# Kernel optimization log

Hardware: AMD Instinct MI355X
Metric: run time of the kernel (lower is better)

Reference implementation:

```python
import jax, jax.numpy as jnp
import numpy as np

B, L, H, W = 16, 4096, 64, 64
SEQ = 1024  # target_sequence_length (hardcoded in the torch module)
SP = 32     # sqrt(SEQ)


def _conv1d(x, w, b, pad):
    y = jax.lax.conv_general_dilated(x, w, (1,), [(pad, pad)],
                                     dimension_numbers=('NCH', 'OIH', 'NCH'))
    return y + b[None, :, None]


def _conv2d(x, w, b, pad, groups=1):
    y = jax.lax.conv_general_dilated(x, w, (1, 1), [(pad, pad)] * 2,
                                     feature_group_count=groups,
                                     dimension_numbers=('NCHW', 'OIHW', 'NCHW'))
    return y + b[None, :, None, None]


def _forward(us_input, img_input, us_w1, us_b1, us_w2, us_b2, us_w3, us_b3,
             aff_w, aff_w_high, aff_thr, img_w1, img_b1, img_w2, img_b2, img_w3, img_b3,
             db_qkv_w, db_qkv_b, db_dw_w, db_dw_b, db_proj_w, db_proj_b,
             db_fc_w, db_fc_b, db_dep_w, db_dep_b, db_temp,
             ca_qkv_w, ca_qkv_b, ca_out_w, ca_out_b,
             tf_ch1_w, tf_ch1_b, tf_ch2_w, tf_ch2_b,
             tf_sp1_w, tf_sp1_b, tf_sp2_w, tf_sp2_b, cls_w, cls_b):
    b = us_input.shape[0]
    # ---- ultrasound 1D conv branch ----
    x = us_input.transpose(0, 2, 1)                    # [B,1,L]
    x = jax.nn.relu(_conv1d(x, us_w1, us_b1, 1))
    x = jax.nn.relu(_conv1d(x, us_w2, us_b2, 1))
    x = jax.nn.relu(_conv1d(x, us_w3, us_b3, 1))
    us_feat = x.transpose(0, 2, 1)                     # [B,L,64]
    # ---- adaptive frequency filtering (training-mode high-freq mask included) ----
    n = us_feat.shape[1]
    xf = jnp.fft.rfft(us_feat, axis=1, norm='ortho')   # [B,Nf,64] complex
    w_c = aff_w[:, 0] + 1j * aff_w[:, 1]
    xw = xf * w_c
    energy = jnp.sum(jnp.abs(xf) ** 2, axis=-1)        # [B,Nf]
    med = jnp.median(energy.reshape(b, -1), axis=1, keepdims=True)
    ne = energy / (med + 1e-6)
    hard = (ne > aff_thr).astype(jnp.float32)
    mask = jax.lax.stop_gradient(hard - aff_thr) + aff_thr  # straight-through threshold
    wh_c = aff_w_high[:, 0] + 1j * aff_w_high[:, 1]
    xw = xw + (xf * mask[..., None]) * wh_c
    us_feat = jnp.fft.irfft(xw, n=n, axis=1, norm='ortho')  # [B,L,64]
    # ---- image 2D conv branch ----
    y = jax.nn.relu(_conv2d(img_input, img_w1, img_b1, 1))
    y = jax.nn.relu(_conv2d(y, img_w2, img_b2, 1))
    y = jax.nn.relu(_conv2d(y, img_w3, img_b3, 1))     # [B,64,H,W]
    # ---- dual-branch feature fusion block ----
    hgt, wid = y.shape[2], y.shape[3]
    hw = hgt * wid
    qkv = jnp.einsum('oi,bihw->bohw', db_qkv_w, y) + db_qkv_b[None, :, None, None]
    qkv = _conv2d(qkv, db_dw_w, db_dw_b, 1, groups=192)      # depthwise (3x3x3 conv @ D=1 -> center 3x3)
    # convolutional branch: faithful row-major reshape as in torch
    f_all = qkv.reshape(b, hw, 12, 16).transpose(0, 2, 1, 3)  # [B,12,HW,16]
    f_all = jnp.einsum('oi,bink->bonk', db_fc_w, f_all) + db_fc_b[None, :, None, None]
    f_conv = f_all.transpose(0, 3, 1, 2).reshape(b, 144, hgt, wid)
    out_conv = _conv2d(f_conv, db_dep_w, db_dep_b, 1, groups=16)  # [B,64,H,W]
    # channel attention branch
    q, k, v = jnp.split(qkv, 3, axis=1)
    q = q.reshape(b, 4, 16, hw)
    k = k.reshape(b, 4, 16, hw)
    v = v.reshape(b, 4, 16, hw)
    q = q / jnp.maximum(jnp.linalg.norm(q, axis=-1, keepdims=True), 1e-12)
    k = k / jnp.maximum(jnp.linalg.norm(k, axis=-1, keepdims=True), 1e-12)
    attn = jax.nn.softmax(jnp.einsum('bhcn,bhdn->bhcd', q, k) * db_temp, axis=-1)
    out = jnp.einsum('bhcd,bhdn->bhcn', attn, v).reshape(b, 64, hgt, wid)
    out = jnp.einsum('oi,bihw->bohw', db_proj_w, out) + db_proj_b[None, :, None, None]
    img_feat = (out + out_conv).reshape(b, 64, hw).transpose(0, 2, 1)  # [B,HW,64]
    # ---- adaptive avg pool to SEQ (lengths divide evenly) ----
    us_red = us_feat.transpose(0, 2, 1).reshape(b, 64, SEQ, -1).mean(-1).transpose(0, 2, 1)
    img_red = img_feat.transpose(0, 2, 1).reshape(b, 64, SEQ, -1).mean(-1).transpose(0, 2, 1)
    # ---- cross-modal attention (shared qkv/out projections) ----
    def heads(t):
        u = (jnp.einsum('bli,oi->blo', t, ca_qkv_w) + ca_qkv_b).reshape(b, SEQ, 4, 3, 16)
        return (u[:, :, :, 0].transpose(0, 2, 1, 3),
                u[:, :, :, 1].transpose(0, 2, 1, 3),
                u[:, :, :, 2].transpose(0, 2, 1, 3))
    q1, k1, v1 = heads(us_red)
    q2, k2, v2 = heads(img_red)
    scale = 1.0 / jnp.sqrt(jnp.float32(16.0))
    a1 = jax.nn.softmax(jnp.einsum('bhqd,bhkd->bhqk', q1, k2) * scale, axis=-1)
    a2 = jax.nn.softmax(jnp.einsum('bhqd,bhkd->bhqk', q2, k1) * scale, axis=-1)
    o1 = jnp.einsum('bhqk,bhkd->bhqd', a1, v2).transpose(0, 2, 1, 3).reshape(b, SEQ, 64)
    o2 = jnp.einsum('bhqk,bhkd->bhqd', a2, v1).transpose(0, 2, 1, 3).reshape(b, SEQ, 64)
    o1 = jnp.einsum('bli,oi->blo', o1, ca_out_w) + ca_out_b
    o2 = jnp.einsum('bli,oi->blo', o2, ca_out_w) + ca_out_b
    t1 = o1.transpose(0, 2, 1).reshape(b, 64, SP, SP)
    t2 = o2.transpose(0, 2, 1).reshape(b, 64, SP, SP)
    # ---- modal fusion attention (channel + spatial gating) ----
    ch_pool = jnp.stack([t1.mean((2, 3)), t1.max((2, 3)), t2.mean((2, 3)), t2.max((2, 3))], axis=1)  # [B,4,64]
    c1 = _conv1d(ch_pool, tf_ch1_w, tf_ch1_b, 1)      # [B,1,64]
    c2 = _conv1d(ch_pool, tf_ch2_w, tf_ch2_b, 1)
    ch_stack = jax.nn.softmax(jnp.stack([c1, c2], 0), axis=0)      # [2,B,1,64]
    ch_stack = ch_stack.transpose(0, 1, 3, 2)[..., None]           # [2,B,64,1,1]
    sp_pool = jnp.concatenate([t1.mean(1, keepdims=True), t1.max(1, keepdims=True),
                               t2.mean(1, keepdims=True), t2.max(1, keepdims=True)], axis=1)
    s1 = _conv2d(sp_pool, tf_sp1_w, tf_sp1_b, 3)
    s2 = _conv2d(sp_pool, tf_sp2_w, tf_sp2_b, 3)
    sp_stack = jax.nn.softmax(jnp.stack([s1, s2], 0), axis=0)      # [2,B,1,SP,SP]
    att = ch_stack + sp_stack + 1.0                                # [2,B,64,SP,SP]
    fuse = att[0] * t1 + att[1] * t2
    logits = fuse.mean((2, 3)) @ cls_w.T + cls_b
    return jax.nn.softmax(logits, axis=1)


def setup_inputs() -> dict:
    key = jax.random.key(0)
    ks = iter(jax.random.split(key, 64))
    def rn(shape, s=0.2):
        return jax.random.normal(next(ks), shape, dtype=jnp.float32) * s
    d = {
        'us_input': jax.random.normal(next(ks), (B, L, 1), dtype=jnp.float32),
        'img_input': jax.random.normal(next(ks), (B, 3, H, W), dtype=jnp.float32),
        'us_w1': rn((16, 1, 3)), 'us_b1': rn((16,), 0.02),
        'us_w2': rn((32, 16, 3)), 'us_b2': rn((32,), 0.02),
        'us_w3': rn((64, 32, 3)), 'us_b3': rn((64,), 0.02),
        'aff_w': rn((64, 2), 0.02), 'aff_w_high': rn((64, 2), 0.02),
        'aff_thr': jax.random.uniform(next(ks), (1,), dtype=jnp.float32),
        'img_w1': rn((16, 3, 3, 3)), 'img_b1': rn((16,), 0.02),
        'img_w2': rn((32, 16, 3, 3)), 'img_b2': rn((32,), 0.02),
        'img_w3': rn((64, 32, 3, 3)), 'img_b3': rn((64,), 0.02),
        'db_qkv_w': rn((192, 64), 0.1), 'db_qkv_b': rn((192,), 0.02),
        'db_dw_w': rn((192, 1, 3, 3)), 'db_dw_b': rn((192,), 0.02),
        'db_proj_w': rn((64, 64), 0.1), 'db_proj_b': rn((64,), 0.02),
        'db_fc_w': rn((9, 12), 0.1), 'db_fc_b': rn((9,), 0.02),
        'db_dep_w': rn((64, 9, 3, 3), 0.1), 'db_dep_b': rn((64,), 0.02),
        'db_temp': jnp.ones((4, 1, 1), dtype=jnp.float32),
        'ca_qkv_w': rn((192, 64), 0.1), 'ca_qkv_b': rn((192,), 0.02),
        'ca_out_w': rn((64, 64), 0.1), 'ca_out_b': rn((64,), 0.02),
        'tf_ch1_w': rn((1, 4, 3)), 'tf_ch1_b': rn((1,), 0.02),
        'tf_ch2_w': rn((1, 4, 3)), 'tf_ch2_b': rn((1,), 0.02),
        'tf_sp1_w': rn((1, 4, 7, 7)), 'tf_sp1_b': rn((1,), 0.02),
        'tf_sp2_w': rn((1, 4, 7, 7)), 'tf_sp2_b': rn((1,), 0.02),
        'cls_w': rn((9, 64), 0.1), 'cls_b': rn((9,), 0.02),
    }
    return d


def reference(us_input, img_input, us_w1, us_b1, us_w2, us_b2, us_w3, us_b3,
              aff_w, aff_w_high, aff_thr, img_w1, img_b1, img_w2, img_b2, img_w3, img_b3,
              db_qkv_w, db_qkv_b, db_dw_w, db_dw_b, db_proj_w, db_proj_b,
              db_fc_w, db_fc_b, db_dep_w, db_dep_b, db_temp,
              ca_qkv_w, ca_qkv_b, ca_out_w, ca_out_b,
              tf_ch1_w, tf_ch1_b, tf_ch2_w, tf_ch2_b,
              tf_sp1_w, tf_sp1_b, tf_sp2_w, tf_sp2_b, cls_w, cls_b):
    return _forward(us_input, img_input, us_w1, us_b1, us_w2, us_b2, us_w3, us_b3,
                    aff_w, aff_w_high, aff_thr, img_w1, img_b1, img_w2, img_b2, img_w3, img_b3,
                    db_qkv_w, db_qkv_b, db_dw_w, db_dw_b, db_proj_w, db_proj_b,
                    db_fc_w, db_fc_b, db_dep_w, db_dep_b, db_temp,
                    ca_qkv_w, ca_qkv_b, ca_out_w, ca_out_b,
                    tf_ch1_w, tf_ch1_b, tf_ch2_w, tf_ch2_b,
                    tf_sp1_w, tf_sp1_b, tf_sp2_w, tf_sp2_b, cls_w, cls_b)
```

## Files before the change

kernel.cpp:

```cpp
#include <hip/hip_runtime.h>

typedef float v2f __attribute__((ext_vector_type(2)));

static constexpr size_t O_SMALL   = 0;
static constexpr size_t O_US3     = 3145728;
static constexpr size_t O_XF      = 7340032;
static constexpr size_t O_USFILT  = 11536384;
static constexpr size_t O_ENERGY  = 15730688;
static constexpr size_t O_MED     = 15764480;
static constexpr size_t O_NRM     = 15765504;
static constexpr size_t O_ATTNS   = 15767552;
static constexpr size_t O_CHPOOL  = 15783936;
static constexpr size_t O_CHW     = 15788032;
static constexpr size_t O_SPPOOL  = 15790080;
static constexpr size_t O_SPW     = 15855616;
static constexpr size_t O_QKV     = 15888384;
static constexpr size_t O_QKVDW   = 28471296;
static constexpr size_t O_OUTCONV = 41054208;
static constexpr size_t CA_Q1 = 2, CA_K1 = 3, CA_V1 = 4,
                        CA_Q2 = 5, CA_K2 = 6, CA_V2 = 7, CA_O1 = 8, CA_O2 = 9,
                        CA_T1 = 10, CA_T2 = 11;


template<int Ci, int Co>
// ... 116 lines not shown
            float rev = (float)jm * cfac;
            float s1 = __builtin_amdgcn_sinf(rev);
            float c1 = __builtin_amdgcn_cosf(rev);
            float c2 = c1 * c1 - s1 * s1, s2 = 2.f * c1 * s1;
            float c3 = c2 * c1 - s2 * s1, s3 = c2 * s1 + s2 * c1;
            float2 v0 = va[r][0], v1 = va[r][1], v2 = va[r][2], v3 = va[r][3];
            float2 u1 = make_float2(v1.x * c1 - v1.y * s1, v1.x * s1 + v1.y * c1);
            float2 u2 = make_float2(v2.x * c2 - v2.y * s2, v2.x * s2 + v2.y * c2);
            float2 u3 = make_float2(v3.x * c3 - v3.y * s3, v3.x * s3 + v3.y * c3);
            float t0x = v0.x + u2.x, t0y = v0.y + u2.y;
            float t1x = v0.x - u2.x, t1y = v0.y - u2.y;
            float t2x = u1.x + u3.x, t2y = u1.y + u3.y;
            float t3x = u1.x - u3.x, t3y = u1.y - u3.y;
            int base = ((j - jm) << 2) + jm;
            A[base]          = make_float2(t0x + t2x, t0y + t2y);
            A[base + Ns]     = make_float2(t1x + t3y, t1y - t3x);
            A[base + 2 * Ns] = make_float2(t0x - t2x, t0y - t2y);
            A[base + 3 * Ns] = make_float2(t1x - t3y, t1y + t3x);
        }
        __syncthreads();
        Ns <<= 2;
    }
}

__device__ __forceinline__ void fft_fwd_body(char* smem_raw, int row,
    const float* __restrict__ us3, float* __restrict__ xf)
{
    float2* A = (float2*)smem_raw;
    int tid = threadIdx.x;
    const float* x = us3 + (size_t)row * 4096;
    for (int r = 0; r < 16; ++r) {
        int i = (r << 8) + tid;
        A[i] = make_float2(x[i], 0.f);
    }
    __syncthreads();
    fft4096_r4_sb(A, tid);
    float* out = xf + (size_t)row * 4098;
    for (int r = 0; r < 9; ++r) {
        int f = (r << 8) + tid;
        if (f < 2049) {
            out[2 * f]     = A[f].x * (1.f / 64.f);
            out[2 * f + 1] = A[f].y * (1.f / 64.f);
        }
    }
}

__device__ __forceinline__ void energy_body(int bid,
    const float* __restrict__ xf, float* __restrict__ energy)
{
    int idx = bid * 256 + threadIdx.x;
    if (idx >= 16 * 2049) return;
    int b = idx / 2049, f = idx % 2049;
    const float* p = xf + (size_t)b * 64 * 4098 + 2 * f;
    float e = 0.f;
    for (int ch = 0; ch < 64; ++ch) {
        float re = p[0], im = p[1];
        e += re * re + im * im;
        p += 4098;
    }
    energy[idx] = e;
}

__device__ __forceinline__ void median_body(char* smem_raw, int b,
    const float* __restrict__ energy, float* __restrict__ med)
{
    float* s = (float*)smem_raw;
    int tid = threadIdx.x;
    for (int r = 0; r < 16; ++r) {
        int i = (r << 8) + tid;
        s[i] = (i < 2049) ? energy[b * 2049 + i] : 3.0e38f;
    }
    __syncthreads();
    for (int k = 2; k <= 4096; k <<= 1) {
        for (int j = k >> 1; j > 0; j >>= 1) {
            for (int r = 0; r < 16; ++r) {
                int i = (r << 8) + tid;
                int ixj = i ^ j;
                if (ixj > i) {
                    bool up = ((i & k) == 0);
                    float a = s[i], bb = s[ixj];
                    if ((a > bb) == up) { s[i] = bb; s[ixj] = a; }
                }
            }
            __syncthreads();
        }
    }
    if (tid == 0) med[b] = s[1024];
}

__device__ __forceinline__ void filter_ifft_body(char* smem_raw, int row,
    const float* __restrict__ xf, const float* __restrict__ energy,
    const float* __restrict__ med, const float* __restrict__ aff_w,
    const float* __restrict__ aff_wh, const float* __restrict__ thr_p,
    float* __restrict__ us_redT)
{
    float2* A = (float2*)smem_raw;
    int b = row >> 6, ch = row & 63;
    int tid = threadIdx.x;
    float thr = thr_p[0];
    float mden = med[b] + 1e-6f;
    float w0r = aff_w[2 * ch], w0i = aff_w[2 * ch + 1];
    float whr = aff_wh[2 * ch], whi = aff_wh[2 * ch + 1];
    const float* X = xf + (size_t)row * 4098;
    const float* E = energy + b * 2049;
    for (int r = 0; r < 9; ++r) {
        int f = (r << 8) + tid;
        if (f < 2049) {
            float re = X[2 * f], im = X[2 * f + 1];
            float mask = (E[f] / mden > thr) ? 1.f : 0.f;
            float wr = w0r + mask * whr;
            float wi = w0i + mask * whi;
            float xr = re * wr - im * wi;
            float xi = re * wi + im * wr;
            A[f] = make_float2(xr, -xi);
            if (f >= 1 && f <= 2047) A[4096 - f] = make_float2(xr, xi);
        }
    }
    __syncthreads();
    fft4096_r4_sb(A, tid);
    float* outp = us_redT + (size_t)row * 1024;
    const float SCL = 0.25f * (1.f / 64.f);
#pragma unroll
    for (int r = 0; r < 4; ++r) {
        int s4 = (r << 8) + tid;
        float v = (A[4 * s4].x + A[4 * s4 + 1].x + A[4 * s4 + 2].x + A[4 * s4 + 3].x) * SCL;
        outp[s4] = v;
    }
}

__device__ __forceinline__ void qkv1x1_body(int bid, const float* __restrict__ y,
    const float* __restrict__ w, const float* __restrict__ bs, float* __restrict__ out)
{
    int oc = bid & 3;
    int pc = (bid >> 2) & 15;
    int b  = bid >> 6;
    int p = pc * 256 + threadIdx.x;
    const float* inb = y + (size_t)b * 262144 + p;
    v2f reg[32];
#pragma unroll
    for (int ci = 0; ci < 32; ++ci) {
        v2f r; r.x = inb[(2 * ci) * 4096]; r.y = inb[(2 * ci + 1) * 4096];
        reg[ci] = r;
    }
    float* ob = out + (size_t)b * 786432 + (size_t)oc * 48 * 4096 + p;
    for (int o = 0; o < 48; ++o) {
        const v2f* wr = (const v2f*)(w + (oc * 48 + o) * 64);
        v2f s2 = {0.f, 0.f};
#pragma unroll
        for (int ci = 0; ci < 32; ++ci) s2 = wr[ci] * reg[ci] + s2;
        ob[o * 4096] = bs[oc * 48 + o] + s2.x + s2.y;
    }
}

__device__ __forceinline__ void dwconv_body(int bid, const float* __restrict__ in,
    const float* __restrict__ w, const float* __restrict__ bs, float* __restrict__ out)
{
    int idx = bid * 256 + threadIdx.x;
    int x = idx & 63, yy = (idx >> 6) & 63;
    int c = (idx >> 12) % 192;
    const float* p = in + idx;
    const float* wp = w + c * 9;
    float acc = bs[c];
    bool ym = yy > 0, yp = yy < 63, xm = x > 0, xp = x < 63;
    float s = wp[4] * p[0];
    if (ym) { s += wp[1] * p[-64]; if (xm) s += wp[0] * p[-65]; if (xp) s += wp[2] * p[-63]; }
    if (xm) s += wp[3] * p[-1];
    if (xp) s += wp[5] * p[1];
    if (yp) { s += wp[7] * p[64];  if (xm) s += wp[6] * p[63];  if (xp) s += wp[8] * p[65]; }
    out[idx] = acc + s;
}

__device__ __forceinline__ void fc_body(int bid, const float* __restrict__ qkv_dw,
    const float* __restrict__ fw, const float* __restrict__ fb, float* __restrict__ fcv)
{
    int idx = bid * 256 + threadIdx.x;
    int k = idx & 15;
    int p = (idx >> 4) & 4095;
    int b = idx >> 16;
    const float* base = qkv_dw + (size_t)b * 786432;
    float u[12];
#pragma unroll
    for (int i = 0; i < 12; ++i) u[i] = base[p * 192 + i * 16 + k];
#pragma unroll
    for (int o = 0; o < 9; ++o) {
        float s = fb[o];
#pragma unroll
        for (int i = 0; i < 12; ++i) s += fw[o * 12 + i] * u[i];
        fcv[(((size_t)b * 16 + k) * 9 + o) * 4096 + p] = s;
    }
}

__device__ __forceinline__ void depconv2_body(char* smem_raw, int bid,
    const float* __restrict__ fcv, const float* __restrict__ w,
    const float* __restrict__ bs, float* __restrict__ out)
{
    auto lds = (float(*)[10][66])smem_raw;
    int band = bid & 7;
    int g    = (bid >> 3) & 15;
    int b    = bid >> 7;
    int y0 = band * 8;
    int tid = threadIdx.x;
    const float* inb = fcv + ((size_t)(b * 16 + g) * 9) * 4096;
    for (int i = tid; i < 9 * 10 * 64; i += 256) {
        int x  = i & 63;
        int ry = (i >> 6) % 10;
        int ci = i / 640;
        int gy = y0 - 1 + ry;
        lds[ci][ry][x + 1] = (gy >= 0 && gy < 64) ? inb[ci * 4096 + gy * 64 + x] : 0.f;
    }
    for (int i = tid; i < 90; i += 256) {
        int ry = i % 10, ci = i / 10;
        lds[ci][ry][0] = 0.f; lds[ci][ry][65] = 0.f;
    }
    __syncthreads();
    int co   = tid >> 6;
    int ysub = (tid >> 3) & 7;
    int x0   = (tid & 7) * 8;
    int ocg  = g * 4 + co;
    float acc[8];
    float bias = bs[ocg];
#pragma unroll
    for (int j = 0; j < 8; ++j) acc[j] = bias;
    const float* wb = w + ocg * 81;
    for (int ci = 0; ci < 9; ++ci) {
        float wr[9];
#pragma unroll
        for (int k = 0; k < 9; ++k) wr[k] = wb[ci * 9 + k];
#pragma unroll
        for (int dy = 0; dy < 3; ++dy) {
            const float* lr = &lds[ci][ysub + dy][x0];
            float a = lr[0], bb = lr[1];
#pragma unroll
            for (int j = 0; j < 8; ++j) {
                float cc = lr[2 + j];
                acc[j] += wr[dy * 3] * a + wr[dy * 3 + 1] * bb + wr[dy * 3 + 2] * cc;
                a = bb; bb = cc;
            }
        }
    }
    float* ob = out + ((size_t)b * 64 + ocg) * 4096 + (y0 + ysub) * 64 + x0;
#pragma unroll
    for (int j = 0; j < 8; ++j) ob[j] = acc[j];
}

__device__ __forceinline__ void qknorm_body(char* smem_raw, int row,
    const float* __restrict__ qkv_dw, float* __restrict__ nrm)
{
    float* red = (float*)smem_raw;
    int which = row >> 10;
    int r = row & 1023;
    int b = r >> 6, hd = r & 63;
    const float* p = qkv_dw + ((size_t)b * 192 + which * 64 + hd) * 4096;
    float s = 0.f;
    for (int i = threadIdx.x; i < 4096; i += 256) { float v = p[i]; s += v * v; }
    red[threadIdx.x] = s;
    __syncthreads();
    for (int st = 128; st > 0; st >>= 1) {
        if (threadIdx.x < st) red[threadIdx.x] += red[threadIdx.x + st];
        __syncthreads();
    }
    if (threadIdx.x == 0) nrm[row] = sqrtf(red[0]);
}

__device__ __forceinline__ void chan_attn_part_body(char* smem_raw, int blk,
    const float* __restrict__ qkv_dw, float* __restrict__ part)
{
    auto Qs  = (float(*)[130])smem_raw;
    auto Ks2 = (float(*)[130])(smem_raw + 16 * 130 * 4);
    int nc = blk & 7;
    int bh = blk >> 3;
    int b = bh >> 2, h = bh & 3;
    int c = threadIdx.x >> 4, d = threadIdx.x & 15;
    const float* qbase = qkv_dw + ((size_t)b * 192 + h * 16) * 4096 + nc * 512;
    const float* kbase = qkv_dw + ((size_t)b * 192 + 64 + h * 16) * 4096 + nc * 512;
    float s = 0.f;
    for (int n0 = 0; n0 < 512; n0 += 128) {
        __syncthreads();
        for (int r = 0; r < 8; ++r) {
            int i = (r << 8) + threadIdx.x;
            int row = i >> 7, col = i & 127;
            Qs[row][col]  = qbase[(size_t)row * 4096 + n0 + col];
            Ks2[row][col] = kbase[(size_t)row * 4096 + n0 + col];
        }
        __syncthreads();
#pragma unroll 8
        for (int n = 0; n < 128; ++n) s += Qs[c][n] * Ks2[d][n];
    }
    part[(size_t)blk * 256 + threadIdx.x] = s;
}

__device__ __forceinline__ void chpool2_body(int bid, const float* __restrict__ t1,
    const float* __restrict__ t2, float* __restrict__ chpool)
{
    int rg = bid & 15;
    int b  = bid >> 4;
    int wave = threadIdx.x >> 6, lane = threadIdx.x & 63;
    int c = rg * 4 + wave;
    const float* p1 = t1 + ((size_t)b * 64 + c) * 1024;
    const float* p2 = t2 + ((size_t)b * 64 + c) * 1024;
    float m1 = 0.f, x1 = -3e38f, m2 = 0.f, x2 = -3e38f;
#pragma unroll
    for (int i = 0; i < 16; ++i) {
        int p = lane + i * 64;
        float a = p1[p], bb = p2[p];
        m1 += a; x1 = fmaxf(x1, a);
        m2 += bb; x2 = fmaxf(x2, bb);
    }
    for (int off = 32; off > 0; off >>= 1) {
        m1 += __shfl_xor(m1, off);
        x1 = fmaxf(x1, __shfl_xor(x1, off));
        m2 += __shfl_xor(m2, off);
        x2 = fmaxf(x2, __shfl_xor(x2, off));
    }
    if (lane == 0) {
        chpool[b * 256 + c]       = m1 * (1.f / 1024.f);
        chpool[b * 256 + 64 + c]  = x1;
        chpool[b * 256 + 128 + c] = m2 * (1.f / 1024.f);
        chpool[b * 256 + 192 + c] = x2;
    }
}

__device__ __forceinline__ void sppool_body(int bid, const float* __restrict__ t1,
    const float* __restrict__ t2, float* __restrict__ sppool)
{
    int b = bid >> 2;
    int p = (bid & 3) * 256 + threadIdx.x;
    float m1 = 0.f, x1 = -3e38f, m2 = 0.f, x2 = -3e38f;
    const float* p1 = t1 + (size_t)b * 65536 + p;
    const float* p2 = t2 + (size_t)b * 65536 + p;
    for (int c = 0; c < 64; ++c) {
        float a = p1[c * 1024], bb = p2[c * 1024];
        m1 += a; x1 = fmaxf(x1, a);
        m2 += bb; x2 = fmaxf(x2, bb);
    }
    sppool[b * 4096 + p]        = m1 * (1.f / 64.f);
    sppool[b * 4096 + 1024 + p] = x1;
    sppool[b * 4096 + 2048 + p] = m2 * (1.f / 64.f);
    sppool[b * 4096 + 3072 + p] = x2;
}

__device__ __forceinline__ void chgate_body(int b, const float* __restrict__ chpool,
    const float* __restrict__ w1, const float* __restrict__ b1,
    const float* __restrict__ w2, const float* __restrict__ b2, float* __restrict__ chw)
{
    int c = threadIdx.x;
    if (c >= 64) return;
    float a1 = b1[0], a2 = b2[0];
    for (int ic = 0; ic < 4; ++ic) {
        const float* cp = chpool + b * 256 + ic * 64;
        for (int d = -1; d <= 1; ++d) {
            int cc = c + d;
            if (cc >= 0 && cc < 64) {
                a1 += w1[ic * 3 + d + 1] * cp[cc];
                a2 += w2[ic * 3 + d + 1] * cp[cc];
            }
        }
    }
    float mx = fmaxf(a1, a2);
    float e1 = __expf(a1 - mx), e2 = __expf(a2 - mx);
    float inv = 1.f / (e1 + e2);
    chw[b * 64 + c]        = e1 * inv;
    chw[1024 + b * 64 + c] = e2 * inv;
}

__device__ __forceinline__ void spgate_body(int bid, const float* __restrict__ sppool,
    const float* __restrict__ w1, const float* __restrict__ b1,
    const float* __restrict__ w2, const float* __restrict__ b2, float* __restrict__ spw)
{
    int idx = bid * 256 + threadIdx.x;
    int p = idx & 1023;
    int b = idx >> 10;
    int y = p >> 5, x = p & 31;
    float a1 = b1[0], a2 = b2[0];
    for (int ic = 0; ic < 4; ++ic) {
        const float* sp = sppool + b * 4096 + ic * 1024;
        for (int dy = -3; dy <= 3; ++dy) {
            int yy = y + dy;
            if (yy < 0 || yy > 31) continue;
            for (int dx = -3; dx <= 3; ++dx) {
                int xx = x + dx;
                if (xx < 0 || xx > 31) continue;
                float v = sp[yy * 32 + xx];
                int wi = ic * 49 + (dy + 3) * 7 + (dx + 3);
                a1 += w1[wi] * v;
                a2 += w2[wi] * v;
            }
        }
    }
    float mx = fmaxf(a1, a2);
    float e1 = __expf(a1 - mx), e2 = __expf(a2 - mx);
    float inv = 1.f / (e1 + e2);
    spw[idx]         = e1 * inv;
    spw[16384 + idx] = e2 * inv;
}


__global__ __launch_bounds__(256) void s1_kernel(const float* us_in, const float* uw, const float* ub,
    float* uo, const float* iin, const float* iw, const float* ib, float* io)
{
    __shared__ __align__(16) char smem[3168];
    if (blockIdx.x < 512) conv1d3_body<1, 16>(smem, blockIdx.x, us_in, uw, ub, uo);
    else                  conv2d3_body<3, 16, 2>(smem, blockIdx.x - 512, iin, iw, ib, io);
}

__global__ __launch_bounds__(256) void s2_kernel(const float* ui, const float* uw, const float* ub,
    float* uo, const float* ii, const float* iw, const float* ib, float* io)
{
    __shared__ __align__(16) char smem[16896];
    if (blockIdx.x < 512) conv1d3_body<16, 32>(smem, blockIdx.x, ui, uw, ub, uo);
    else                  conv2d3_body<16, 32, 2>(smem, blockIdx.x - 512, ii, iw, ib, io);
}

__global__ __launch_bounds__(256) void s3_kernel(const float* ui, const float* uw, const float* ub,
    float* uo, const float* ii, const float* iw, const float* ib, float* io)
{
    __shared__ __align__(16) char smem[33792];
    if (blockIdx.x < 512) conv1d3_body<32, 64>(smem, blockIdx.x, ui, uw, ub, uo);
    else                  conv2d3_body<32, 64, 2>(smem, blockIdx.x - 512, ii, iw, ib, io);
}

__global__ __launch_bounds__(256) void s4_kernel(const float* us3, float* xf,
    const float* y, const float* qw, const float* qb, float* qkv)
{
    __shared__ __align__(16) char smem[32768];
    if (blockIdx.x < 1024) fft_fwd_body(smem, blockIdx.x, us3, xf);
    else                   qkv1x1_body(blockIdx.x - 1024, y, qw, qb, qkv);
}

__global__ __launch_bounds__(256) void s5_kernel(const float* qkv, const float* dww,
    const float* dwb, float* qkv_dw, const float* xf, float* energy)
{
    if (blockIdx.x < 49152) dwconv_body(blockIdx.x, qkv, dww, dwb, qkv_dw);
    else                    energy_body(blockIdx.x - 49152, xf, energy);
}

__global__ __launch_bounds__(256) void s6_kernel(const float* qkv_dw, const float* fw,
    const float* fb, float* fcv, const float* energy, float* med, float* part)
{
    __shared__ __align__(16) char smem[16640];
    if (blockIdx.x < 4096)      fc_body(blockIdx.x, qkv_dw, fw, fb, fcv);
    else if (blockIdx.x < 4112) median_body(smem, blockIdx.x - 4096, energy, med);
    else                        chan_attn_part_body(smem, blockIdx.x - 4112, qkv_dw, part);
}

__global__ __launch_bounds__(256) void s7_kernel(const float* fcv, const float* dw,
    const float* db, float* out_conv, const float* qkv_dw, float* nrm,
    const float* xf, const float* energy, const float* med, const float* aw,
    const float* awh, const float* thr, float* us_redT)
{
    __shared__ __align__(16) char smem[32768];
    if (blockIdx.x < 2048)      depconv2_body(smem, blockIdx.x, fcv, dw, db, out_conv);
    else if (blockIdx.x < 4096) qknorm_body(smem, blockIdx.x - 2048, qkv_dw, nrm);
    else                        filter_ifft_body(smem, blockIdx.x - 4096, xf, energy, med, aw, awh, thr, us_redT);
}

__global__ __launch_bounds__(256) void zero_kernel(float* o1t, float* o2t, float* lsg,
                                                   unsigned* kmax2)
{
    int idx = blockIdx.x * 256 + threadIdx.x;
    if (idx < 1048576) { o1t[idx] = 0.f; o2t[idx] = 0.f; }
    if (idx < 131072) lsg[idx] = 0.f;
    if (idx < 128) kmax2[idx] = 0u;
}

__global__ __launch_bounds__(256) void s16_kernel(const float* t1, const float* t2,
    float* chpool, float* sppool)
{
    if (blockIdx.x < 256) chpool2_body(blockIdx.x, t1, t2, chpool);
    else                  sppool_body(blockIdx.x - 256, t1, t2, sppool);
}

__global__ __launch_bounds__(256) void s17_kernel(const float* sppool, const float* sw1,
    const float* sb1, const float* sw2, const float* sb2, float* spw,
    const float* chpool, const float* cw1, const float* cb1, const float* cw2,
    const float* cb2, float* chw)
{
    if (blockIdx.x < 64) spgate_body(blockIdx.x, sppool, sw1, sb1, sw2, sb2, spw);
    else                 chgate_body(blockIdx.x - 64, chpool, cw1, cb1, cw2, cb2, chw);
}

__global__ __launch_bounds__(256) void chan_attn_merge_kernel(
    const float* __restrict__ part, const float* __restrict__ nrm,
    const float* __restrict__ temp, float* __restrict__ attn_s)
{
    int bh = blockIdx.x;
    int b = bh >> 2, h = bh & 3;
    int c = threadIdx.x >> 4, d = threadIdx.x & 15;
    float s = 0.f;
#pragma unroll
    for (int i = 0; i < 8; ++i) s += part[(size_t)(bh * 8 + i) * 256 + threadIdx.x];
    float nq = fmaxf(nrm[b * 64 + h * 16 + c], 1e-12f);
    float nk = fmaxf(nrm[1024 + b * 64 + h * 16 + d], 1e-12f);
    s = s / (nq * nk) * temp[h];
    __shared__ float S[16][17];
    S[c][d] = s;
    __syncthreads();
    if (threadIdx.x < 16) {
        int cc = threadIdx.x;
        float mx = -3e30f;
        for (int dd = 0; dd < 16; ++dd) mx = fmaxf(mx, S[cc][dd]);
        float sm = 0.f;
        float e[16];
        for (int dd = 0; dd < 16; ++dd) { e[dd] = __expf(S[cc][dd] - mx); sm += e[dd]; }
        float inv = 1.f / sm;
        float* dst = attn_s + (size_t)bh * 256 + cc * 16;
        for (int dd = 0; dd < 16; ++dd) dst[dd] = e[dd] * inv;
    }
}


__global__ __launch_bounds__(256, 2) void attnproj_kernel(const float* __restrict__ attn_s,
    const float* __restrict__ qkv_dw, const float* __restrict__ outconv,
    const float* __restrict__ pw, const float* __restrict__ pb, float* __restrict__ img_feat)
{
    int blk = blockIdx.x;
    int oc = blk & 1;
    int pc = (blk >> 1) & 15;
    int b  = blk >> 5;
    int n = pc * 256 + threadIdx.x;
    const float* vb = qkv_dw + ((size_t)b * 192 + 128) * 4096 + n;
    v2f v[32];
#pragma unroll
    for (int i = 0; i < 32; ++i) {
        v2f r; r.x = vb[(2 * i) * 4096]; r.y = vb[(2 * i + 1) * 4096];
        v[i] = r;
    }
    const float* ab = attn_s + (size_t)b * 1024;
    for (int h = 0; h < 4; ++h) {
        v2f tmp[8];
#pragma unroll
        for (int c2 = 0; c2 < 8; ++c2) {
            v2f s2a = {0.f, 0.f}, s2b = {0.f, 0.f};
            const v2f* r0 = (const v2f*)(ab + (h * 16 + 2 * c2) * 16);
            const v2f* r1 = (const v2f*)(ab + (h * 16 + 2 * c2 + 1) * 16);
#pragma unroll
            for (int d2 = 0; d2 < 8; ++d2) {
                s2a = r0[d2] * v[h * 8 + d2] + s2a;
                s2b = r1[d2] * v[h * 8 + d2] + s2b;
            }
            v2f t; t.x = s2a.x + s2a.y; t.y = s2b.x + s2b.y;
            tmp[c2] = t;
        }
#pragma unroll
        for (int c2 = 0; c2 < 8; ++c2) v[h * 8 + c2] = tmp[c2];
    }
    float* ofb = img_feat + (size_t)b * 262144 + (size_t)oc * 32 * 4096 + n;
    const float* ocb = outconv + (size_t)b * 262144 + (size_t)oc * 32 * 4096 + n;
    for (int o = 0; o < 32; ++o) {
        const v2f* wr = (const v2f*)(pw + (oc * 32 + o) * 64);
        v2f s2 = {0.f, 0.f};
#pragma unroll
        for (int c2 = 0; c2 < 32; ++c2) s2 = wr[c2] * v[c2] + s2;
        ofb[o * 4096] = pb[oc * 32 + o] + ocb[o * 4096] + s2.x + s2.y;
    }
}

__global__ __launch_bounds__(256) void poolred_img_kernel(const float* __restrict__ img_feat,
    float* __restrict__ img_redT)
{
    int idx = blockIdx.x * 256 + threadIdx.x;
    int s4 = idx & 1023;
    int bc = idx >> 10;
    const float* in = img_feat + (size_t)bc * 4096 + s4 * 4;
    float4 v4 = *(const float4*)in;
    img_redT[(size_t)bc * 1024 + s4] = 0.25f * (v4.x + v4.y + v4.z + v4.w);
}

__global__ __launch_bounds__(256, 2) void caqkv2_kernel(const float* __restrict__ us_redT,
    const float* __restrict__ img_redT, const float* __restrict__ qw, const float* __restrict__ qb,
    float* __restrict__ q1, float* __restrict__ k1, float* __restrict__ v1,
    float* __restrict__ q2, float* __restrict__ k2, float* __restrict__ v2,
    unsigned* __restrict__ kmax2)
{
    int blk = blockIdx.x;
    int h  = blk & 3;
    int pc = (blk >> 2) & 3;
    int b  = (blk >> 4) & 15;
    int m  = blk >> 8;
    int l = pc * 256 + threadIdx.x;
    const float* in = (m ? img_redT : us_redT) + (size_t)b * 65536 + l;
    v2f reg[32];
#pragma unroll
    for (int i = 0; i < 32; ++i) {
        v2f r; r.x = in[(2 * i) * 1024]; r.y = in[(2 * i + 1) * 1024];
        reg[i] = r;
    }
    size_t rowoff = ((size_t)(b * 4 + h) * 1024 + l) * 16;
    float* dst[3] = { (m ? q2 : q1) + rowoff, (m ? k2 : k1) + rowoff, (m ? v2 : v1) + rowoff };
    float knorm2 = 0.f;
#pragma unroll
    for (int which = 0; which < 3; ++which) {
        float* dp = dst[which];
        for (int d = 0; d < 16; ++d) {
            int o = h * 48 + which * 16 + d;
            const v2f* wr = (const v2f*)(qw + o * 64);
            v2f s2 = {0.f, 0.f};
#pragma unroll
            for (int i = 0; i < 32; ++i) s2 = wr[i] * reg[i] + s2;
            float val = qb[o] + s2.x + s2.y;
            dp[d] = val;
            if (which == 1) knorm2 += val * val;
        }
    }
    for (int off = 32; off > 0; off >>= 1)
        knorm2 = fmaxf(knorm2, __shfl_xor(knorm2, off));
    if ((threadIdx.x & 63) == 0) {
        int unit = b * 8 + (1 - m) * 4 + h;
        atomicMax(&kmax2[unit], __float_as_uint(knorm2));
    }
}

__global__ __launch_bounds__(256, 2) void cross_attn9_kernel(
    const float* __restrict__ q1, const float* __restrict__ k1, const float* __restrict__ v1,
    const float* __restrict__ q2, const float* __restrict__ k2, const float* __restrict__ v2,
    const unsigned* __restrict__ kmax2, float* __restrict__ ls_glob,
    float* __restrict__ o1t, float* __restrict__ o2t)
{
    int blk  = blockIdx.x;
    int kt   = blk & 7;
    int unit = blk >> 3;
    int h = unit & 3;
    int m = (unit >> 2) & 1;
    int b = unit >> 3;
    const float* Q = m ? q2 : q1;
    const float* K = m ? k1 : k2;
    const float* V = m ? v1 : v2;
    const float* Qb = Q + (size_t)(b * 4 + h) * 16384;
    const float* Kb = K + (size_t)(b * 4 + h) * 16384 + kt * 128 * 16;
    const float* Vb = V + (size_t)(b * 4 + h) * 16384 + kt * 128 * 16;
    int tid = threadIdx.x;
    const float SC = 0.25f * 1.44269504088896340736f;
    float km = sqrtf(__uint_as_float(kmax2[unit]));
    v2f qr[4][8], acc[4][8];
    float M[4], ls[4];
#pragma unroll
    for (int j = 0; j < 4; ++j) {
        const v2f* qp = (const v2f*)(Qb + (size_t)(tid + 256 * j) * 16);
        v2f qs2 = {0.f, 0.f};
#pragma unroll
        for (int i = 0; i < 8; ++i) {
            v2f q = qp[i];
            qs2 = q * q + qs2;
            qr[j][i] = q * SC;
        }
        M[j] = sqrtf(qs2.x + qs2.y) * km * SC;
        ls[j] = 0.f;
#pragma unroll
        for (int i = 0; i < 8; ++i) acc[j][i] = (v2f){0.f, 0.f};
    }
    __shared__ float Ks[64 * 16];
    __shared__ float Vs[64 * 16];
    for (int t0 = 0; t0 < 128; t0 += 64) {
        __syncthreads();
        ((float4*)Ks)[tid] = ((const float4*)(Kb + t0 * 16))[tid];
        ((float4*)Vs)[tid] = ((const float4*)(Vb + t0 * 16))[tid];
        __syncthreads();
#pragma unroll 2
        for (int t = 0; t < 64; ++t) {
            const v2f* k2p = (const v2f*)&Ks[t * 16];
            v2f kk[8];
// ... 34 lines not shown
    }
}

__global__ __launch_bounds__(256, 2) void caout3_kernel(const float* __restrict__ o1t,
    const float* __restrict__ o2t, const float* __restrict__ ls_glob,
    const float* __restrict__ ow, const float* __restrict__ ob_,
    float* __restrict__ t1, float* __restrict__ t2)
{
    int blk = blockIdx.x;
    int oc = blk & 1;
    int pc = (blk >> 1) & 3;
    int b  = (blk >> 3) & 15;
    int m  = blk >> 7;
    int l = pc * 256 + threadIdx.x;
    float inv[4];
#pragma unroll
    for (int h = 0; h < 4; ++h)
        inv[h] = 1.f / ls_glob[(size_t)(b * 8 + m * 4 + h) * 1024 + l];
    const float* in = (m ? o2t : o1t) + (size_t)b * 65536 + l;
    v2f reg[32];
#pragma unroll
    for (int i = 0; i < 32; ++i) {
        float iv = inv[i >> 3];
        v2f r; r.x = in[(2 * i) * 1024] * iv; r.y = in[(2 * i + 1) * 1024] * iv;
        reg[i] = r;
    }
    float* t = (m ? t2 : t1) + (size_t)b * 65536 + (size_t)oc * 32 * 1024 + l;
    for (int o = 0; o < 32; ++o) {
        const v2f* wr = (const v2f*)(ow + (oc * 32 + o) * 64);
        v2f s2 = {0.f, 0.f};
#pragma unroll
        for (int i = 0; i < 32; ++i) s2 = wr[i] * reg[i] + s2;
        t[o * 1024] = ob_[oc * 32 + o] + s2.x + s2.y;
    }
}

__global__ __launch_bounds__(256) void final2_kernel(const float* __restrict__ t1,
    const float* __restrict__ t2, const float* __restrict__ chw, const float* __restrict__ spw,
    const float* __restrict__ clsw, const float* __restrict__ clsb, float* __restrict__ out)
{
    int b = blockIdx.x;
    int wave = threadIdx.x >> 6, lane = threadIdx.x & 63;
    __shared__ float feat[64];
    __shared__ float lg[9];
    const float* s1 = spw + b * 1024;
    const float* s2 = spw + 16384 + b * 1024;
    for (int round = 0; round < 16; ++round) {
        int c = round * 4 + wave;
        float g1 = chw[b * 64 + c] + 1.f;
        float g2 = chw[1024 + b * 64 + c] + 1.f;
        const float* p1 = t1 + ((size_t)b * 64 + c) * 1024;
        const float* p2 = t2 + ((size_t)b * 64 + c) * 1024;
        float acc = 0.f;
#pragma unroll
        for (int i = 0; i < 16; ++i) {
            int p = lane + i * 64;
            acc += (g1 + s1[p]) * p1[p] + (g2 + s2[p]) * p2[p];
        }
        for (int off = 32; off > 0; off >>= 1) acc += __shfl_xor(acc, off);
        if (lane == 0) feat[c] = acc * (1.f / 1024.f);
    }
    __syncthreads();
    if (threadIdx.x < 9) {
        int c = threadIdx.x;
        float s = clsb[c];
        for (int i = 0; i < 64; ++i) s += clsw[c * 64 + i] * feat[i];
        lg[c] = s;
    }
    __syncthreads();
    if (threadIdx.x == 0) {
        float mx = -3e38f;
        for (int o = 0; o < 9; ++o) mx = fmaxf(mx, lg[o]);
        float sm = 0.f;
        float e[9];
        for (int o = 0; o < 9; ++o) { e[o] = __expf(lg[o] - mx); sm += e[o]; }
        float inv = 1.f / sm;
        for (int o = 0; o < 9; ++o) out[b * 9 + o] = e[o] * inv;
    }
}

extern "C" void kernel_launch(void* const* d_in, const int* in_sizes, int n_in,
                              void* d_out, int out_size, void* d_ws, size_t ws_size,
                              hipStream_t stream)
{
    (void)in_sizes; (void)n_in; (void)out_size; (void)ws_size;
    const float* us_input = (const float*)d_in[0];
    const float* img_input = (const float*)d_in[1];
    const float* us_w1 = (const float*)d_in[2];  const float* us_b1 = (const float*)d_in[3];
    const float* us_w2 = (const float*)d_in[4];  const float* us_b2 = (const float*)d_in[5];
    const float* us_w3 = (const float*)d_in[6];  const float* us_b3 = (const float*)d_in[7];
    const float* aff_w = (const float*)d_in[8];  const float* aff_wh = (const float*)d_in[9];
    const float* aff_thr = (const float*)d_in[10];
    const float* img_w1 = (const float*)d_in[11]; const float* img_b1 = (const float*)d_in[12];
    const float* img_w2 = (const float*)d_in[13]; const float* img_b2 = (const float*)d_in[14];
    const float* img_w3 = (const float*)d_in[15]; const float* img_b3 = (const float*)d_in[16];
    const float* db_qkv_w = (const float*)d_in[17]; const float* db_qkv_b = (const float*)d_in[18];
    const float* db_dw_w = (const float*)d_in[19];  const float* db_dw_b = (const float*)d_in[20];
    const float* db_proj_w = (const float*)d_in[21]; const float* db_proj_b = (const float*)d_in[22];
    const float* db_fc_w = (const float*)d_in[23];  const float* db_fc_b = (const float*)d_in[24];
    const float* db_dep_w = (const float*)d_in[25]; const float* db_dep_b = (const float*)d_in[26];
    const float* db_temp = (const float*)d_in[27];
    const float* ca_qkv_w = (const float*)d_in[28]; const float* ca_qkv_b = (const float*)d_in[29];
    const float* ca_out_w = (const float*)d_in[30]; const float* ca_out_b = (const float*)d_in[31];
    const float* tf_ch1_w = (const float*)d_in[32]; const float* tf_ch1_b = (const float*)d_in[33];
    const float* tf_ch2_w = (const float*)d_in[34]; const float* tf_ch2_b = (const float*)d_in[35];
    const float* tf_sp1_w = (const float*)d_in[36]; const float* tf_sp1_b = (const float*)d_in[37];
    const float* tf_sp2_w = (const float*)d_in[38]; const float* tf_sp2_b = (const float*)d_in[39];
    const float* cls_w = (const float*)d_in[40];   const float* cls_b = (const float*)d_in[41];

    float* ws = (float*)d_ws;
    float* us1     = ws + O_SMALL;
    float* us2     = ws + O_SMALL + 1048576;
    float* us3     = ws + O_US3;
    float* xf      = ws + O_XF;
    float* energy  = ws + O_ENERGY;
    float* med     = ws + O_MED;
    float* nrm     = ws + O_NRM;
    float* attn_s  = ws + O_ATTNS;
    float* chpool  = ws + O_CHPOOL;
    float* chw     = ws + O_CHW;
    float* sppool  = ws + O_SPPOOL;
    float* spw     = ws + O_SPW;
    float* qkv     = ws + O_QKV;
    float* qkv_dw  = ws + O_QKVDW;
    float* out_conv= ws + O_OUTCONV;
    float* img1 = ws + O_USFILT;
    float* img2 = ws + O_USFILT + 1048576;
    float* y = ws + O_QKVDW;
    float* fcv = qkv;
    float* img_feat = xf;
    float* ca_part = ws + O_SMALL;
    float* ca_ls    = ws + O_US3;
    unsigned* ca_kmax2 = (unsigned*)(ws + O_US3 + 131072);
    float* us_redT  = ws + O_US3 + 262144;
    float* img_redT = ws + O_US3 + 1310720;
    float* q1 = ws + O_QKV + CA_Q1 * 1048576;
    float* k1 = ws + O_QKV + CA_K1 * 1048576;
    float* v1 = ws + O_QKV + CA_V1 * 1048576;
    float* q2 = ws + O_QKV + CA_Q2 * 1048576;
    float* k2 = ws + O_QKV + CA_K2 * 1048576;
    float* v2 = ws + O_QKV + CA_V2 * 1048576;
    float* o1t = ws + O_QKV + CA_O1 * 1048576;
    float* o2t = ws + O_QKV + CA_O2 * 1048576;
    float* t1 = ws + O_QKV + CA_T1 * 1048576;
    float* t2 = ws + O_QKV + CA_T2 * 1048576;

    s1_kernel<<<1024, 256, 0, stream>>>(us_input, us_w1, us_b1, us1,
                                        img_input, img_w1, img_b1, img1);
    s2_kernel<<<1024, 256, 0, stream>>>(us1, us_w2, us_b2, us2,
                                        img1, img_w2, img_b2, img2);
    s3_kernel<<<1024, 256, 0, stream>>>(us2, us_w3, us_b3, us3,
                                        img2, img_w3, img_b3, y);
    s4_kernel<<<2048, 256, 0, stream>>>(us3, xf, y, db_qkv_w, db_qkv_b, qkv);
    s5_kernel<<<49281, 256, 0, stream>>>(qkv, db_dw_w, db_dw_b, qkv_dw, xf, energy);
    s6_kernel<<<4624, 256, 0, stream>>>(qkv_dw, db_fc_w, db_fc_b, fcv, energy, med, ca_part);
    s7_kernel<<<5120, 256, 0, stream>>>(fcv, db_dep_w, db_dep_b, out_conv,
                                        qkv_dw, nrm, xf, energy, med,
                                        aff_w, aff_wh, aff_thr, us_redT);
    zero_kernel<<<4096, 256, 0, stream>>>(o1t, o2t, ca_ls, ca_kmax2);
    chan_attn_merge_kernel<<<64, 256, 0, stream>>>(ca_part, nrm, db_temp, attn_s);
    attnproj_kernel<<<512, 256, 0, stream>>>(attn_s, qkv_dw, out_conv, db_proj_w, db_proj_b, img_feat);
    poolred_img_kernel<<<4096, 256, 0, stream>>>(img_feat, img_redT);
    caqkv2_kernel<<<512, 256, 0, stream>>>(us_redT, img_redT, ca_qkv_w, ca_qkv_b,
                                           q1, k1, v1, q2, k2, v2, ca_kmax2);
    cross_attn9_kernel<<<1024, 256, 0, stream>>>(q1, k1, v1, q2, k2, v2, ca_kmax2,
                                                 ca_ls, o1t, o2t);
    caout3_kernel<<<256, 256, 0, stream>>>(o1t, o2t, ca_ls, ca_out_w, ca_out_b, t1, t2);
    s16_kernel<<<320, 256, 0, stream>>>(t1, t2, chpool, sppool);
    s17_kernel<<<80, 256, 0, stream>>>(sppool, tf_sp1_w, tf_sp1_b, tf_sp2_w, tf_sp2_b, spw,
                                       chpool, tf_ch1_w, tf_ch1_b, tf_ch2_w, tf_ch2_b, chw);
    final2_kernel<<<16, 256, 0, stream>>>(t1, t2, chw, spw, cls_w, cls_b, (float*)d_out);
}
```

Baseline: 858.8 us.

## Tile depthwise 3x3 conv through LDS and merge zero/attn-merge launches

The depthwise 3x3 conv now runs one block per (batch, channel) plane. Each block stages a zero-padded 66x66 tile in shared memory, and each thread computes 16 outputs from registers with sliding reuse, replacing the one-output-per-thread version that issued masked global loads. Separately, the zero-init kernel and the channel-attention merge kernel are combined into a single launch to remove one dispatch. The cost is about 17 KB of LDS per block in s5 and fewer, heavier blocks. Those blocks share the launch with the energy blocks.

After: 832.4 us. 1.03x faster.

```diff
diff --git a/kernel.cpp b/kernel.cpp
--- a/kernel.cpp
+++ b/kernel.cpp
@@ -292,22 +292,46 @@
     }
 }
 
-__device__ __forceinline__ void dwconv_body(int bid, const float* __restrict__ in,
-    const float* __restrict__ w, const float* __restrict__ bs, float* __restrict__ out)
-{
-    int idx = bid * 256 + threadIdx.x;
-    int x = idx & 63, yy = (idx >> 6) & 63;
-    int c = (idx >> 12) % 192;
-    const float* p = in + idx;
-    const float* wp = w + c * 9;
-    float acc = bs[c];
-    bool ym = yy > 0, yp = yy < 63, xm = x > 0, xp = x < 63;
-    float s = wp[4] * p[0];
-    if (ym) { s += wp[1] * p[-64]; if (xm) s += wp[0] * p[-65]; if (xp) s += wp[2] * p[-63]; }
-    if (xm) s += wp[3] * p[-1];
-    if (xp) s += wp[5] * p[1];
-    if (yp) { s += wp[7] * p[64];  if (xm) s += wp[6] * p[63];  if (xp) s += wp[8] * p[65]; }
-    out[idx] = acc + s;
+__device__ __forceinline__ void dwconv2_body(char* smem_raw, int bid,
+    const float* __restrict__ in, const float* __restrict__ w,
+    const float* __restrict__ bs, float* __restrict__ out)
+{
+    auto lds = (float(*)[66])smem_raw;
+    int c = bid % 192;
+    int b = bid / 192;
+    int tid = threadIdx.x;
+    const float* inb = in + ((size_t)b * 192 + c) * 4096;
+    for (int i = tid; i < 66 * 64; i += 256) {
+        int col = i & 63;
+        int row = i >> 6;
+        int gy = row - 1;
+        lds[row][col + 1] = (gy >= 0 && gy < 64) ? inb[gy * 64 + col] : 0.f;
+    }
+    for (int r = tid; r < 66; r += 256) { lds[r][0] = 0.f; lds[r][65] = 0.f; }
+    __syncthreads();
+    float wr[9];
+#pragma unroll
+    for (int k = 0; k < 9; ++k) wr[k] = w[c * 9 + k];
+    float bias = bs[c];
+    int y  = tid >> 2;
+    int x0 = (tid & 3) * 16;
+    float acc[16];
+#pragma unroll
+    for (int j = 0; j < 16; ++j) acc[j] = bias;
+#pragma unroll
+    for (int dy = 0; dy < 3; ++dy) {
+        const float* lr = &lds[y + dy][x0];
+        float a = lr[0], bb = lr[1];
+#pragma unroll
+        for (int j = 0; j < 16; ++j) {
+            float cc = lr[2 + j];
+            acc[j] += wr[dy * 3] * a + wr[dy * 3 + 1] * bb + wr[dy * 3 + 2] * cc;
+            a = bb; bb = cc;
+        }
+    }
+    float* ob = out + ((size_t)b * 192 + c) * 4096 + y * 64 + x0;
+#pragma unroll
+    for (int j = 0; j < 16; ++j) ob[j] = acc[j];
 }
 
 __device__ __forceinline__ void fc_body(int bid, const float* __restrict__ qkv_dw,
@@ -534,96 +558,20 @@
     spw[16384 + idx] = e2 * inv;
 }
 
-
-__global__ __launch_bounds__(256) void s1_kernel(const float* us_in, const float* uw, const float* ub,
-    float* uo, const float* iin, const float* iw, const float* ib, float* io)
-{
-    __shared__ __align__(16) char smem[3168];
-    if (blockIdx.x < 512) conv1d3_body<1, 16>(smem, blockIdx.x, us_in, uw, ub, uo);
-    else                  conv2d3_body<3, 16, 2>(smem, blockIdx.x - 512, iin, iw, ib, io);
-}
-
-__global__ __launch_bounds__(256) void s2_kernel(const float* ui, const float* uw, const float* ub,
-    float* uo, const float* ii, const float* iw, const float* ib, float* io)
-{
-    __shared__ __align__(16) char smem[16896];
-    if (blockIdx.x < 512) conv1d3_body<16, 32>(smem, blockIdx.x, ui, uw, ub, uo);
-    else                  conv2d3_body<16, 32, 2>(smem, blockIdx.x - 512, ii, iw, ib, io);
-}
-
-__global__ __launch_bounds__(256) void s3_kernel(const float* ui, const float* uw, const float* ub,
-    float* uo, const float* ii, const float* iw, const float* ib, float* io)
-{
-    __shared__ __align__(16) char smem[33792];
-    if (blockIdx.x < 512) conv1d3_body<32, 64>(smem, blockIdx.x, ui, uw, ub, uo);
-    else                  conv2d3_body<32, 64, 2>(smem, blockIdx.x - 512, ii, iw, ib, io);
-}
-
-__global__ __launch_bounds__(256) void s4_kernel(const float* us3, float* xf,
-    const float* y, const float* qw, const float* qb, float* qkv)
-{
-    __shared__ __align__(16) char smem[32768];
-    if (blockIdx.x < 1024) fft_fwd_body(smem, blockIdx.x, us3, xf);
-    else                   qkv1x1_body(blockIdx.x - 1024, y, qw, qb, qkv);
-}
-
-__global__ __launch_bounds__(256) void s5_kernel(const float* qkv, const float* dww,
-    const float* dwb, float* qkv_dw, const float* xf, float* energy)
-{
-    if (blockIdx.x < 49152) dwconv_body(blockIdx.x, qkv, dww, dwb, qkv_dw);
-    else                    energy_body(blockIdx.x - 49152, xf, energy);
-}
-
-__global__ __launch_bounds__(256) void s6_kernel(const float* qkv_dw, const float* fw,
-    const float* fb, float* fcv, const float* energy, float* med, float* part)
-{
-    __shared__ __align__(16) char smem[16640];
-    if (blockIdx.x < 4096)      fc_body(blockIdx.x, qkv_dw, fw, fb, fcv);
-    else if (blockIdx.x < 4112) median_body(smem, blockIdx.x - 4096, energy, med);
-    else                        chan_attn_part_body(smem, blockIdx.x - 4112, qkv_dw, part);
-}
-
-__global__ __launch_bounds__(256) void s7_kernel(const float* fcv, const float* dw,
-    const float* db, float* out_conv, const float* qkv_dw, float* nrm,
-    const float* xf, const float* energy, const float* med, const float* aw,
-    const float* awh, const float* thr, float* us_redT)
-{
-    __shared__ __align__(16) char smem[32768];
-    if (blockIdx.x < 2048)      depconv2_body(smem, blockIdx.x, fcv, dw, db, out_conv);
-    else if (blockIdx.x < 4096) qknorm_body(smem, blockIdx.x - 2048, qkv_dw, nrm);
-    else                        filter_ifft_body(smem, blockIdx.x - 4096, xf, energy, med, aw, awh, thr, us_redT);
-}
-
-__global__ __launch_bounds__(256) void zero_kernel(float* o1t, float* o2t, float* lsg,
-                                                   unsigned* kmax2)
-{
-    int idx = blockIdx.x * 256 + threadIdx.x;
+__device__ __forceinline__ void zero_body(int bid, float* o1t, float* o2t, float* lsg,
+                                          unsigned* kmax2)
+{
+    int idx = bid * 256 + threadIdx.x;
     if (idx < 1048576) { o1t[idx] = 0.f; o2t[idx] = 0.f; }
     if (idx < 131072) lsg[idx] = 0.f;
     if (idx < 128) kmax2[idx] = 0u;
 }
 
-__global__ __launch_bounds__(256) void s16_kernel(const float* t1, const float* t2,
-    float* chpool, float* sppool)
-{
-    if (blockIdx.x < 256) chpool2_body(blockIdx.x, t1, t2, chpool);
-    else                  sppool_body(blockIdx.x - 256, t1, t2, sppool);
-}
-
-__global__ __launch_bounds__(256) void s17_kernel(const float* sppool, const float* sw1,
-    const float* sb1, const float* sw2, const float* sb2, float* spw,
-    const float* chpool, const float* cw1, const float* cb1, const float* cw2,
-    const float* cb2, float* chw)
-{
-    if (blockIdx.x < 64) spgate_body(blockIdx.x, sppool, sw1, sb1, sw2, sb2, spw);
-    else                 chgate_body(blockIdx.x - 64, chpool, cw1, cb1, cw2, cb2, chw);
-}
-
-__global__ __launch_bounds__(256) void chan_attn_merge_kernel(
+__device__ __forceinline__ void chan_attn_merge_body(int bh,
     const float* __restrict__ part, const float* __restrict__ nrm,
     const float* __restrict__ temp, float* __restrict__ attn_s)
 {
-    int bh = blockIdx.x;
+    __shared__ float S[16][17];
     int b = bh >> 2, h = bh & 3;
     int c = threadIdx.x >> 4, d = threadIdx.x & 15;
     float s = 0.f;
@@ -632,7 +580,6 @@
     float nq = fmaxf(nrm[b * 64 + h * 16 + c], 1e-12f);
     float nk = fmaxf(nrm[1024 + b * 64 + h * 16 + d], 1e-12f);
     s = s / (nq * nk) * temp[h];
-    __shared__ float S[16][17];
     S[c][d] = s;
     __syncthreads();
     if (threadIdx.x < 16) {
@@ -646,6 +593,90 @@
         float* dst = attn_s + (size_t)bh * 256 + cc * 16;
         for (int dd = 0; dd < 16; ++dd) dst[dd] = e[dd] * inv;
     }
+}
+
+
+__global__ __launch_bounds__(256) void s1_kernel(const float* us_in, const float* uw, const float* ub,
+    float* uo, const float* iin, const float* iw, const float* ib, float* io)
+{
+    __shared__ __align__(16) char smem[3168];
+    if (blockIdx.x < 512) conv1d3_body<1, 16>(smem, blockIdx.x, us_in, uw, ub, uo);
+    else                  conv2d3_body<3, 16, 2>(smem, blockIdx.x - 512, iin, iw, ib, io);
+}
+
+__global__ __launch_bounds__(256) void s2_kernel(const float* ui, const float* uw, const float* ub,
+    float* uo, const float* ii, const float* iw, const float* ib, float* io)
+{
+    __shared__ __align__(16) char smem[16896];
+    if (blockIdx.x < 512) conv1d3_body<16, 32>(smem, blockIdx.x, ui, uw, ub, uo);
+    else                  conv2d3_body<16, 32, 2>(smem, blockIdx.x - 512, ii, iw, ib, io);
+}
+
+__global__ __launch_bounds__(256) void s3_kernel(const float* ui, const float* uw, const float* ub,
+    float* uo, const float* ii, const float* iw, const float* ib, float* io)
+{
+    __shared__ __align__(16) char smem[33792];
+    if (blockIdx.x < 512) conv1d3_body<32, 64>(smem, blockIdx.x, ui, uw, ub, uo);
+    else                  conv2d3_body<32, 64, 2>(smem, blockIdx.x - 512, ii, iw, ib, io);
+}
+
+__global__ __launch_bounds__(256) void s4_kernel(const float* us3, float* xf,
+    const float* y, const float* qw, const float* qb, float* qkv)
+{
+    __shared__ __align__(16) char smem[32768];
+    if (blockIdx.x < 1024) fft_fwd_body(smem, blockIdx.x, us3, xf);
+    else                   qkv1x1_body(blockIdx.x - 1024, y, qw, qb, qkv);
+}
+
+__global__ __launch_bounds__(256) void s5_kernel(const float* qkv, const float* dww,
+    const float* dwb, float* qkv_dw, const float* xf, float* energy)
+{
+    __shared__ __align__(16) char smem[66 * 66 * 4];
+    if (blockIdx.x < 3072) dwconv2_body(smem, blockIdx.x, qkv, dww, dwb, qkv_dw);
+    else                   energy_body(blockIdx.x - 3072, xf, energy);
+}
+
+__global__ __launch_bounds__(256) void s6_kernel(const float* qkv_dw, const float* fw,
+    const float* fb, float* fcv, const float* energy, float* med, float* part)
+{
+    __shared__ __align__(16) char smem[16640];
+    if (blockIdx.x < 4096)      fc_body(blockIdx.x, qkv_dw, fw, fb, fcv);
+    else if (blockIdx.x < 4112) median_body(smem, blockIdx.x - 4096, energy, med);
+    else                        chan_attn_part_body(smem, blockIdx.x - 4112, qkv_dw, part);
+}
+
+__global__ __launch_bounds__(256) void s7_kernel(const float* fcv, const float* dw,
+    const float* db, float* out_conv, const float* qkv_dw, float* nrm,
+    const float* xf, const float* energy, const float* med, const float* aw,
+    const float* awh, const float* thr, float* us_redT)
+{
+    __shared__ __align__(16) char smem[32768];
+    if (blockIdx.x < 2048)      depconv2_body(smem, blockIdx.x, fcv, dw, db, out_conv);
+    else if (blockIdx.x < 4096) qknorm_body(smem, blockIdx.x - 2048, qkv_dw, nrm);
+    else                        filter_ifft_body(smem, blockIdx.x - 4096, xf, energy, med, aw, awh, thr, us_redT);
+}
+
+__global__ __launch_bounds__(256) void zm_kernel(float* o1t, float* o2t, float* lsg,
+    unsigned* kmax2, const float* part, const float* nrm, const float* temp, float* attn_s)
+{
+    if (blockIdx.x < 4096) zero_body(blockIdx.x, o1t, o2t, lsg, kmax2);
+    else                   chan_attn_merge_body(blockIdx.x - 4096, part, nrm, temp, attn_s);
+}
+
+__global__ __launch_bounds__(256) void s16_kernel(const float* t1, const float* t2,
+    float* chpool, float* sppool)
+{
+    if (blockIdx.x < 256) chpool2_body(blockIdx.x, t1, t2, chpool);
+    else                  sppool_body(blockIdx.x - 256, t1, t2, sppool);
+}
+
+__global__ __launch_bounds__(256) void s17_kernel(const float* sppool, const float* sw1,
+    const float* sb1, const float* sw2, const float* sb2, float* spw,
+    const float* chpool, const float* cw1, const float* cb1, const float* cw2,
+    const float* cb2, float* chw)
+{
+    if (blockIdx.x < 64) spgate_body(blockIdx.x, sppool, sw1, sb1, sw2, sb2, spw);
+    else                 chgate_body(blockIdx.x - 64, chpool, cw1, cb1, cw2, cb2, chw);
 }
 
 
@@ -986,13 +1017,13 @@
     s3_kernel<<<1024, 256, 0, stream>>>(us2, us_w3, us_b3, us3,
                                         img2, img_w3, img_b3, y);
     s4_kernel<<<2048, 256, 0, stream>>>(us3, xf, y, db_qkv_w, db_qkv_b, qkv);
-    s5_kernel<<<49281, 256, 0, stream>>>(qkv, db_dw_w, db_dw_b, qkv_dw, xf, energy);
+    s5_kernel<<<3201, 256, 0, stream>>>(qkv, db_dw_w, db_dw_b, qkv_dw, xf, energy);
     s6_kernel<<<4624, 256, 0, stream>>>(qkv_dw, db_fc_w, db_fc_b, fcv, energy, med, ca_part);
     s7_kernel<<<5120, 256, 0, stream>>>(fcv, db_dep_w, db_dep_b, out_conv,
                                         qkv_dw, nrm, xf, energy, med,
                                         aff_w, aff_wh, aff_thr, us_redT);
-    zero_kernel<<<4096, 256, 0, stream>>>(o1t, o2t, ca_ls, ca_kmax2);
-    chan_attn_merge_kernel<<<64, 256, 0, stream>>>(ca_part, nrm, db_temp, attn_s);
+    zm_kernel<<<4160, 256, 0, stream>>>(o1t, o2t, ca_ls, ca_kmax2,
+                                        ca_part, nrm, db_temp, attn_s);
     attnproj_kernel<<<512, 256, 0, stream>>>(attn_s, qkv_dw, out_conv, db_proj_w, db_proj_b, img_feat);
     poolred_img_kernel<<<4096, 256, 0, stream>>>(img_feat, img_redT);
     caqkv2_kernel<<<512, 256, 0, stream>>>(us_redT, img_redT, ca_qkv_w, ca_qkv_b,
```
